# Optimization experiments

Measured on AMD Instinct MI355X. Metric: run time of the kernel, lower is better.

## Reference

```python
import jax, jax.numpy as jnp
import numpy as np

DIM = 64
N_ITER = 2
NUM_USR = 50000
NUM_ENT = 200000
NUM_REL = 32
N_NEIGHBOR = 16
BATCH = 4096


def setup_inputs() -> dict:
    key = jax.random.key(0)
    ks = jax.random.split(key, 12)
    u = jax.random.randint(ks[0], (BATCH,), 0, NUM_USR)
    v = jax.random.randint(ks[1], (BATCH,), 0, NUM_ENT)
    adj = jax.random.randint(ks[2], (NUM_ENT, N_NEIGHBOR), 0, NUM_ENT)
    rel_adj = jax.random.randint(ks[3], (NUM_ENT, N_NEIGHBOR), 0, NUM_REL + 1)
    usr_emb = jax.random.normal(ks[4], (NUM_USR, DIM), dtype=jnp.float32)
    ent_emb = jax.random.normal(ks[5], (NUM_ENT, DIM), dtype=jnp.float32)
    rel_emb = jax.random.normal(ks[6], (NUM_REL + 1, DIM), dtype=jnp.float32)
    # per-hop aggregator Linear(dim, dim) weights (applied as x @ W + b)
    scale = 1.0 / np.sqrt(DIM)
    W0 = jax.random.uniform(ks[7], (DIM, DIM), jnp.float32, -scale, scale)
    b0 = jax.random.uniform(ks[8], (DIM,), jnp.float32, -scale, scale)
    W1 = jax.random.uniform(ks[9], (DIM, DIM), jnp.float32, -scale, scale)
    b1 = jax.random.uniform(ks[10], (DIM,), jnp.float32, -scale, scale)
    return {"u": u, "v": v, "adj": adj, "rel_adj": rel_adj,
            "usr_emb": usr_emb, "ent_emb": ent_emb, "rel_emb": rel_emb,
            "W0": W0, "b0": b0, "W1": W1, "b1": b1}


def reference(u, v, adj, rel_adj, usr_emb, ent_emb, rel_emb, W0, b0, W1, b1):
    B = u.shape[0]
    user = usr_emb[u]  # [B, D]

    # multi-hop neighbor index expansion
    entities = [v[:, None]]            # hop h: [B, n^h]
    relations = []
    for h in range(N_ITER):
        ne = adj[entities[h]].reshape(B, -1)      # [B, n^(h+1)]
        nr = rel_adj[entities[h]].reshape(B, -1)
        entities.append(ne)
        relations.append(nr)

    ent_vecs = [ent_emb[e] for e in entities]     # [B, n^h, D]
    rel_vecs = [rel_emb[r] for r in relations]

    Ws, bs = [W0, W1], [b0, b1]
    for i in range(N_ITER):
        act = jnp.tanh if i == N_ITER - 1 else jax.nn.sigmoid
        nxt = []
        for hop in range(N_ITER - i):
            sv = ent_vecs[hop]                                        # [B, m, D]
            nv = ent_vecs[hop + 1].reshape(B, -1, N_NEIGHBOR, DIM)    # [B, m, n, D]
            nr = rel_vecs[hop].reshape(B, -1, N_NEIGHBOR, DIM)        # [B, m, n, D]
            # user-relation attention over neighbors
            scores = jnp.einsum('bd,bmnd->bmn', user, nr)
            attn = jax.nn.softmax(scores, axis=-1)
            agg = jnp.einsum('bmn,bmnd->bmd', attn, nv)
            out = act((sv + agg) @ Ws[i] + bs[i])
            nxt.append(out)
        ent_vecs = nxt

    item = ent_vecs[0].reshape(B, DIM)
    return jax.nn.sigmoid(jnp.sum(user * item, axis=1))
```

## Files before the change

### kernel.cpp

```cpp
#include <hip/hip_runtime.h>

#define DIMN 64
#define NNB 16
#define NREL 33
#define WPB 4

__device__ __forceinline__ float bcastf(float x, int lane) {
    return __int_as_float(__builtin_amdgcn_readlane(__float_as_int(x), lane));
}

__global__ __launch_bounds__(64 * WPB, 4)
void kgs_kernel(const int* __restrict__ u, const int* __restrict__ v,
                const int* __restrict__ adj, const int* __restrict__ rel_adj,
                const float* __restrict__ usr_emb, const float* __restrict__ ent_emb,
                const float* __restrict__ rel_emb,
                const float* __restrict__ W0, const float* __restrict__ b0,
                const float* __restrict__ W1, const float* __restrict__ b1,
                float* __restrict__ out, int B)
{
    const int tid = threadIdx.x;
    const int wid = tid >> 6;
    const int d   = tid & 63;
    int b = blockIdx.x * WPB + wid;
    if (b >= B) b = B - 1;
    const int n16 = d & 15;

    __shared__ __align__(16) float user_sh[WPB][DIMN];
    __shared__ float ur_sh[WPB][NREL + 7];

    const int uu = u[b];
    const int vv = v[b];

    const float user_d = usr_emb[uu * DIMN + d];
    user_sh[wid][d] = user_d;
    __syncthreads();

    if (d < NREL) {
        const float* re = rel_emb + d * DIMN;
        float acc = 0.f;
        #pragma unroll
        for (int k = 0; k < DIMN; k += 4) {
            const float4 uk = *(const float4*)(&user_sh[wid][k]);
            const float4 rk = *(const float4*)(re + k);
            acc = fmaf(uk.x, rk.x, acc);
            acc = fmaf(uk.y, rk.y, acc);
            acc = fmaf(uk.z, rk.z, acc);
            acc = fmaf(uk.w, rk.w, acc);
        }
        ur_sh[wid][d] = acc;
    }
    __syncthreads();

    const int e1n = adj[vv * NNB + n16];
    const int r1n = rel_adj[vv * NNB + n16];
    const float b0d = b0[d];

    float sv_r[NNB];
    float xs[NNB];

    #pragma unroll
    for (int m = 0; m < NNB; ++m) {
        const int em = __builtin_amdgcn_readlane(e1n, m);
        const float sv = ent_emb[em * DIMN + d];

        const int e2n = adj[em * NNB + n16];
        const int r2n = rel_adj[em * NNB + n16];

        const float e = __expf(ur_sh[wid][r2n]);
        float sum = e;
        sum += __shfl_xor(sum, 1);
        sum += __shfl_xor(sum, 2);
        sum += __shfl_xor(sum, 4);
        sum += __shfl_xor(sum, 8);
        const float attn = e * __builtin_amdgcn_rcpf(sum);

        float agg = 0.f;
        #pragma unroll
        for (int n = 0; n < NNB; ++n) {
            const int en = __builtin_amdgcn_readlane(e2n, n);
            agg = fmaf(bcastf(attn, n), ent_emb[en * DIMN + d], agg);
        }
        sv_r[m] = sv;
        xs[m]   = sv + agg;
    }

    float o[NNB];
    #pragma unroll
    for (int m = 0; m < NNB; ++m) o[m] = b0d;

    #pragma unroll 4
    for (int k = 0; k < DIMN; ++k) {
        const float wk = W0[k * DIMN + d];
        #pragma unroll
        for (int m = 0; m < NNB; ++m)
            o[m] = fmaf(bcastf(xs[m], k), wk, o[m]);
    }

    float h1[NNB];
    #pragma unroll
    for (int m = 0; m < NNB; ++m)
        h1[m] = 1.f / (1.f + __expf(-o[m]));

    const float sv0 = ent_emb[vv * DIMN + d];
    const float e0 = __expf(ur_sh[wid][r1n]);
    float sum0 = e0;
    sum0 += __shfl_xor(sum0, 1);
    sum0 += __shfl_xor(sum0, 2);
    sum0 += __shfl_xor(sum0, 4);
    sum0 += __shfl_xor(sum0, 8);
    const float attn0 = e0 * __builtin_amdgcn_rcpf(sum0);

    float agg0 = 0.f, agg1 = 0.f;
    #pragma unroll
    for (int n = 0; n < NNB; ++n) {
        const float an = bcastf(attn0, n);
        agg0 = fmaf(an, sv_r[n], agg0);
        agg1 = fmaf(an, h1[n],  agg1);
    }

    const float x0 = sv0 + agg0;
    {
        float a0 = 0.f, a1 = 0.f, a2 = 0.f, a3 = 0.f;
        for (int k = 0; k < DIMN; k += 4) {
            const float* wr = W0 + k * DIMN;
            a0 = fmaf(bcastf(x0, k + 0), wr[d], a0);
            a1 = fmaf(bcastf(x0, k + 1), wr[DIMN + d], a1);
            a2 = fmaf(bcastf(x0, k + 2), wr[2 * DIMN + d], a2);
            a3 = fmaf(bcastf(x0, k + 3), wr[3 * DIMN + d], a3);
        }
        const float o0 = b0d + ((a0 + a1) + (a2 + a3));
        const float h0 = 1.f / (1.f + __expf(-o0));

        const float x1 = h0 + agg1;
        float c0 = 0.f, c1 = 0.f, c2 = 0.f, c3 = 0.f;
        for (int k = 0; k < DIMN; k += 4) {
            const float* wr = W1 + k * DIMN;
            c0 = fmaf(bcastf(x1, k + 0), wr[d], c0);
            c1 = fmaf(bcastf(x1, k + 1), wr[DIMN + d], c1);
            c2 = fmaf(bcastf(x1, k + 2), wr[2 * DIMN + d], c2);
            c3 = fmaf(bcastf(x1, k + 3), wr[3 * DIMN + d], c3);
        }
        const float o1 = b1[d] + ((c0 + c1) + (c2 + c3));
        const float item_d = 1.f - 2.f / (1.f + __expf(2.f * o1));

        float p = user_d * item_d;
        p += __shfl_xor(p, 1);
        p += __shfl_xor(p, 2);
        p += __shfl_xor(p, 4);
        p += __shfl_xor(p, 8);
        p += __shfl_xor(p, 16);
        p += __shfl_xor(p, 32);
        if (d == 0) out[b] = 1.f / (1.f + __expf(-p));
    }
}

extern "C" void kernel_launch(void* const* d_in, const int* in_sizes, int n_in,
                              void* d_out, int out_size, void* d_ws, size_t ws_size,
                              hipStream_t stream) {
    const int*   u       = (const int*)d_in[0];
    const int*   v       = (const int*)d_in[1];
    const int*   adj     = (const int*)d_in[2];
    const int*   rel_adj = (const int*)d_in[3];
    const float* usr_emb = (const float*)d_in[4];
    const float* ent_emb = (const float*)d_in[5];
    const float* rel_emb = (const float*)d_in[6];
    const float* W0      = (const float*)d_in[7];
    const float* b0      = (const float*)d_in[8];
    const float* W1      = (const float*)d_in[9];
    const float* b1      = (const float*)d_in[10];
    float* out = (float*)d_out;

    const int B = in_sizes[0];
    const int grid = (B + WPB - 1) / WPB;
    kgs_kernel<<<dim3(grid), dim3(64 * WPB), 0, stream>>>(u, v, adj, rel_adj, usr_emb,
                                                          ent_emb, rel_emb, W0, b0, W1, b1,
                                                          out, B);
}
```

Measured before the change: 175.4 us.

## Compute hop-1 W0 projection with split-bf16 MFMA and batch neighbor index loads

A small prep kernel packs W0 into bf16 hi/lo MFMA B-fragments in the workspace. The main kernel stages the 16x64 hop-1 inputs in LDS and computes the projection with three bf16 MFMA passes (hi*hi, hi*lo, lo*hi) to keep near-fp32 accuracy. This replaces the readlane-broadcast FMA loop. The gather phase is also split so all second-hop indices and source rows load before aggregation, which exposes more memory-level parallelism, and the block-wide barriers are dropped because each wave only touches its own LDS rows. In exchange the change adds an extra kernel launch, LDS traffic, and register pressure.

```diff
diff --git a/kernel.cpp b/kernel.cpp
--- a/kernel.cpp
+++ b/kernel.cpp
@@ -4,9 +4,33 @@
 #define NNB 16
 #define NREL 33
 #define WPB 4
+#define XSTR 68
+
+typedef float  floatx4 __attribute__((ext_vector_type(4)));
+typedef short  shortx8 __attribute__((ext_vector_type(8)));
 
 __device__ __forceinline__ float bcastf(float x, int lane) {
     return __int_as_float(__builtin_amdgcn_readlane(__float_as_int(x), lane));
+}
+
+__global__ void prep_w0_frags(const float* __restrict__ W0, unsigned short* __restrict__ wsp) {
+    const int tid = blockIdx.x * blockDim.x + threadIdx.x;
+    if (tid >= 512) return;
+    const int l = tid & 63;
+    const int t = (tid >> 6) & 3;
+    const int ks = tid >> 8;
+    const int k0 = ks * 32 + (l >> 4) * 8;
+    const int n  = t * 16 + (l & 15);
+    const unsigned base = ((unsigned)(ks * 4 + t) * 64 + l) * 8;
+    #pragma unroll
+    for (int j = 0; j < 8; ++j) {
+        const float x = W0[(k0 + j) * DIMN + n];
+        const unsigned u  = __float_as_uint(x);
+        const unsigned uh = u & 0xFFFF0000u;
+        const float lf = x - __uint_as_float(uh);
+        wsp[base + j]        = (unsigned short)(u >> 16);
+        wsp[4096 + base + j] = (unsigned short)(__float_as_uint(lf) >> 16);
+    }
 }
 
 __global__ __launch_bounds__(64 * WPB, 4)
@@ -16,6 +40,7 @@
                 const float* __restrict__ rel_emb,
                 const float* __restrict__ W0, const float* __restrict__ b0,
                 const float* __restrict__ W1, const float* __restrict__ b1,
+                const unsigned short* __restrict__ wsp,
                 float* __restrict__ out, int B)
 {
     const int tid = threadIdx.x;
@@ -27,13 +52,15 @@
 
     __shared__ __align__(16) float user_sh[WPB][DIMN];
     __shared__ float ur_sh[WPB][NREL + 7];
+    __shared__ __align__(16) float xbuf[WPB][NNB * XSTR];
 
     const int uu = u[b];
     const int vv = v[b];
 
     const float user_d = usr_emb[uu * DIMN + d];
+    const int e1n = adj[vv * NNB + n16];
+    const int r1n = rel_adj[vv * NNB + n16];
     user_sh[wid][d] = user_d;
-    __syncthreads();
 
     if (d < NREL) {
         const float* re = rel_emb + d * DIMN;
@@ -49,59 +76,104 @@
         }
         ur_sh[wid][d] = acc;
     }
-    __syncthreads();
-
-    const int e1n = adj[vv * NNB + n16];
-    const int r1n = rel_adj[vv * NNB + n16];
-    const float b0d = b0[d];
 
     float sv_r[NNB];
-    float xs[NNB];
-
+    int   e2n_r[NNB], r2n_r[NNB];
     #pragma unroll
     for (int m = 0; m < NNB; ++m) {
         const int em = __builtin_amdgcn_readlane(e1n, m);
-        const float sv = ent_emb[em * DIMN + d];
-
-        const int e2n = adj[em * NNB + n16];
-        const int r2n = rel_adj[em * NNB + n16];
-
-        const float e = __expf(ur_sh[wid][r2n]);
-        float sum = e;
-        sum += __shfl_xor(sum, 1);
-        sum += __shfl_xor(sum, 2);
-        sum += __shfl_xor(sum, 4);
-        sum += __shfl_xor(sum, 8);
-        const float attn = e * __builtin_amdgcn_rcpf(sum);
-
-        float agg = 0.f;
+        sv_r[m]  = ent_emb[(size_t)em * DIMN + d];
+        e2n_r[m] = adj[em * NNB + n16];
+        r2n_r[m] = rel_adj[em * NNB + n16];
+    }
+
+    float attn[NNB];
+    #pragma unroll
+    for (int m = 0; m < NNB; ++m) {
+        const float e = __expf(ur_sh[wid][r2n_r[m]]);
+        float s = e;
+        s += __shfl_xor(s, 1);
+        s += __shfl_xor(s, 2);
+        s += __shfl_xor(s, 4);
+        s += __shfl_xor(s, 8);
+        attn[m] = e * __builtin_amdgcn_rcpf(s);
+    }
+
+    float agg[NNB];
+    #pragma unroll
+    for (int m = 0; m < NNB; ++m) agg[m] = 0.f;
+    #pragma unroll
+    for (int m = 0; m < NNB; ++m) {
         #pragma unroll
         for (int n = 0; n < NNB; ++n) {
-            const int en = __builtin_amdgcn_readlane(e2n, n);
-            agg = fmaf(bcastf(attn, n), ent_emb[en * DIMN + d], agg);
-        }
-        sv_r[m] = sv;
-        xs[m]   = sv + agg;
-    }
-
-    float o[NNB];
-    #pragma unroll
-    for (int m = 0; m < NNB; ++m) o[m] = b0d;
-
-    #pragma unroll 4
-    for (int k = 0; k < DIMN; ++k) {
-        const float wk = W0[k * DIMN + d];
-        #pragma unroll
-        for (int m = 0; m < NNB; ++m)
-            o[m] = fmaf(bcastf(xs[m], k), wk, o[m]);
-    }
-
-    float h1[NNB];
+            const int en = __builtin_amdgcn_readlane(e2n_r[m], n);
+            const float* rp = ent_emb + (size_t)en * DIMN;
+            agg[m] = fmaf(bcastf(attn[m], n), rp[d], agg[m]);
+        }
+    }
+
     #pragma unroll
     for (int m = 0; m < NNB; ++m)
-        h1[m] = 1.f / (1.f + __expf(-o[m]));
-
-    const float sv0 = ent_emb[vv * DIMN + d];
+        xbuf[wid][m * XSTR + d] = sv_r[m] + agg[m];
+
+    shortx8 Ahi[2], Alo[2];
+    #pragma unroll
+    for (int ks = 0; ks < 2; ++ks) {
+        const float* ar = &xbuf[wid][(d & 15) * XSTR + ((d >> 4) * 8) + ks * 32];
+        const floatx4 xa = *(const floatx4*)ar;
+        const floatx4 xb = *(const floatx4*)(ar + 4);
+        unsigned uh[8], ul[8];
+        #pragma unroll
+        for (int j = 0; j < 8; ++j) {
+            const float x = (j < 4) ? xa[j] : xb[j - 4];
+            const unsigned ub = __float_as_uint(x);
+            uh[j] = ub & 0xFFFF0000u;
+            ul[j] = __float_as_uint(x - __uint_as_float(uh[j]));
+        }
+        union { int i[4]; shortx8 s; } ch, cl;
+        #pragma unroll
+        for (int p = 0; p < 4; ++p) {
+            ch.i[p] = (int)(uh[2 * p + 1] | (uh[2 * p] >> 16));
+            cl.i[p] = (int)((ul[2 * p + 1] & 0xFFFF0000u) | (ul[2 * p] >> 16));
+        }
+        Ahi[ks] = ch.s;
+        Alo[ks] = cl.s;
+    }
+
+    const shortx8* wf = (const shortx8*)wsp;
+    floatx4 acc[4];
+    #pragma unroll
+    for (int t = 0; t < 4; ++t) acc[t] = (floatx4){0.f, 0.f, 0.f, 0.f};
+    #pragma unroll
+    for (int t = 0; t < 4; ++t) {
+        #pragma unroll
+        for (int ks = 0; ks < 2; ++ks) {
+            const int f = ks * 4 + t;
+            const shortx8 bhi = wf[f * 64 + d];
+            const shortx8 blo = wf[512 + f * 64 + d];
+            acc[t] = __builtin_amdgcn_mfma_f32_16x16x32_bf16(Ahi[ks], bhi, acc[t], 0, 0, 0);
+            acc[t] = __builtin_amdgcn_mfma_f32_16x16x32_bf16(Ahi[ks], blo, acc[t], 0, 0, 0);
+            acc[t] = __builtin_amdgcn_mfma_f32_16x16x32_bf16(Alo[ks], bhi, acc[t], 0, 0, 0);
+        }
+    }
+
+    #pragma unroll
+    for (int t = 0; t < 4; ++t) {
+        const float bv = b0[t * 16 + (d & 15)];
+        #pragma unroll
+        for (int reg = 0; reg < 4; ++reg) {
+            const float o = acc[t][reg] + bv;
+            const float h = 1.f / (1.f + __expf(-o));
+            const int m = (d >> 4) * 4 + reg;
+            xbuf[wid][m * XSTR + t * 16 + (d & 15)] = h;
+        }
+    }
+    float h1_r[NNB];
+    #pragma unroll
+    for (int n = 0; n < NNB; ++n)
+        h1_r[n] = xbuf[wid][n * XSTR + d];
+
+    const float sv0 = ent_emb[(size_t)vv * DIMN + d];
     const float e0 = __expf(ur_sh[wid][r1n]);
     float sum0 = e0;
     sum0 += __shfl_xor(sum0, 1);
@@ -115,43 +187,41 @@
     for (int n = 0; n < NNB; ++n) {
         const float an = bcastf(attn0, n);
         agg0 = fmaf(an, sv_r[n], agg0);
-        agg1 = fmaf(an, h1[n],  agg1);
+        agg1 = fmaf(an, h1_r[n], agg1);
     }
 
     const float x0 = sv0 + agg0;
-    {
-        float a0 = 0.f, a1 = 0.f, a2 = 0.f, a3 = 0.f;
-        for (int k = 0; k < DIMN; k += 4) {
-            const float* wr = W0 + k * DIMN;
-            a0 = fmaf(bcastf(x0, k + 0), wr[d], a0);
-            a1 = fmaf(bcastf(x0, k + 1), wr[DIMN + d], a1);
-            a2 = fmaf(bcastf(x0, k + 2), wr[2 * DIMN + d], a2);
-            a3 = fmaf(bcastf(x0, k + 3), wr[3 * DIMN + d], a3);
-        }
-        const float o0 = b0d + ((a0 + a1) + (a2 + a3));
-        const float h0 = 1.f / (1.f + __expf(-o0));
-
-        const float x1 = h0 + agg1;
-        float c0 = 0.f, c1 = 0.f, c2 = 0.f, c3 = 0.f;
-        for (int k = 0; k < DIMN; k += 4) {
-            const float* wr = W1 + k * DIMN;
-            c0 = fmaf(bcastf(x1, k + 0), wr[d], c0);
-            c1 = fmaf(bcastf(x1, k + 1), wr[DIMN + d], c1);
-            c2 = fmaf(bcastf(x1, k + 2), wr[2 * DIMN + d], c2);
-            c3 = fmaf(bcastf(x1, k + 3), wr[3 * DIMN + d], c3);
-        }
-        const float o1 = b1[d] + ((c0 + c1) + (c2 + c3));
-        const float item_d = 1.f - 2.f / (1.f + __expf(2.f * o1));
-
-        float p = user_d * item_d;
-        p += __shfl_xor(p, 1);
-        p += __shfl_xor(p, 2);
-        p += __shfl_xor(p, 4);
-        p += __shfl_xor(p, 8);
-        p += __shfl_xor(p, 16);
-        p += __shfl_xor(p, 32);
-        if (d == 0) out[b] = 1.f / (1.f + __expf(-p));
-    }
+    float a0 = 0.f, a1 = 0.f, a2 = 0.f, a3 = 0.f;
+    for (int k = 0; k < DIMN; k += 4) {
+        const float* wr = W0 + k * DIMN;
+        a0 = fmaf(bcastf(x0, k + 0), wr[d], a0);
+        a1 = fmaf(bcastf(x0, k + 1), wr[DIMN + d], a1);
+        a2 = fmaf(bcastf(x0, k + 2), wr[2 * DIMN + d], a2);
+        a3 = fmaf(bcastf(x0, k + 3), wr[3 * DIMN + d], a3);
+    }
+    const float o0 = b0[d] + ((a0 + a1) + (a2 + a3));
+    const float h0 = 1.f / (1.f + __expf(-o0));
+
+    const float x1 = h0 + agg1;
+    float c0 = 0.f, c1 = 0.f, c2 = 0.f, c3 = 0.f;
+    for (int k = 0; k < DIMN; k += 4) {
+        const float* wr = W1 + k * DIMN;
+        c0 = fmaf(bcastf(x1, k + 0), wr[d], c0);
+        c1 = fmaf(bcastf(x1, k + 1), wr[DIMN + d], c1);
+        c2 = fmaf(bcastf(x1, k + 2), wr[2 * DIMN + d], c2);
+        c3 = fmaf(bcastf(x1, k + 3), wr[3 * DIMN + d], c3);
+    }
+    const float o1 = b1[d] + ((c0 + c1) + (c2 + c3));
+    const float item_d = 1.f - 2.f / (1.f + __expf(2.f * o1));
+
+    float p = user_d * item_d;
+    p += __shfl_xor(p, 1);
+    p += __shfl_xor(p, 2);
+    p += __shfl_xor(p, 4);
+    p += __shfl_xor(p, 8);
+    p += __shfl_xor(p, 16);
+    p += __shfl_xor(p, 32);
+    if (d == 0) out[b] = 1.f / (1.f + __expf(-p));
 }
 
 extern "C" void kernel_launch(void* const* d_in, const int* in_sizes, int n_in,
@@ -169,10 +239,12 @@
     const float* W1      = (const float*)d_in[9];
     const float* b1      = (const float*)d_in[10];
     float* out = (float*)d_out;
+    unsigned short* wsp = (unsigned short*)d_ws;
 
     const int B = in_sizes[0];
+    prep_w0_frags<<<dim3(2), dim3(256), 0, stream>>>(W0, wsp);
     const int grid = (B + WPB - 1) / WPB;
     kgs_kernel<<<dim3(grid), dim3(64 * WPB), 0, stream>>>(u, v, adj, rel_adj, usr_emb,
                                                           ent_emb, rel_emb, W0, b0, W1, b1,
-                                                          out, B);
-}
+                                                          wsp, out, B);
+}
```

Result: faster. 160.4 us (-8.5%).
